# Performance work log

Measured on AMD Instinct MI355X. Metric: run time of the kernel, lower is better.

The kernel has to match this reference:

```python
import jax, jax.numpy as jnp
import numpy as np

LOCAL_HEADS = 8
GLOBAL_HEADS = 4
HEAD_DIM = 16  # dim // local_heads


def setup_inputs() -> dict:
    key = jax.random.key(0)
    ks = jax.random.split(key, 6)
    B, N, C = 8, 1024, 128
    gdim = HEAD_DIM * GLOBAL_HEADS  # 64
    return {
        "x": jax.random.normal(ks[0], (B, N, C), dtype=jnp.float32),
        "masks": jax.random.uniform(ks[1], (N, N, 3), dtype=jnp.float32),
        "Wq": jax.random.normal(ks[2], (gdim, C), dtype=jnp.float32) * 0.05,
        "Wk": jax.random.normal(ks[3], (gdim, C), dtype=jnp.float32) * 0.05,
        "Wv": jax.random.normal(ks[4], (C, C), dtype=jnp.float32) * 0.05,
        "mask_proj": jax.random.normal(ks[5], (3, GLOBAL_HEADS * LOCAL_HEADS), dtype=jnp.float32),
    }


def reference(x, masks, Wq, Wk, Wv, mask_proj):
    B, N, C = x.shape
    # projections (torch Linear: y = x @ W.T)
    q = (x @ Wq.T).reshape(B, N, GLOBAL_HEADS, HEAD_DIM)   # [B,N,G,hd]
    k = (x @ Wk.T).reshape(B, N, GLOBAL_HEADS, HEAD_DIM)
    v = (x @ Wv.T).reshape(B, N, LOCAL_HEADS, HEAD_DIM)    # [B,N,L,hd]
    # raw global-head scores: [B,G,N,N]  (no 1/sqrt(d) scaling in original)
    attn = jnp.einsum('bigd,bjgd->bgij', q, k)
    # learned mask mixing: masks [N,N,3] @ mask_proj [3, G*L] -> [N,N,G,L]
    mw = (masks @ mask_proj).reshape(N, N, GLOBAL_HEADS, LOCAL_HEADS)
    # mix global heads into local heads: [B,L,N,N]
    scores = jnp.einsum('bgij,ijgl->blij', attn, mw)
    probs = jax.nn.softmax(scores, axis=-1)               # over keys j
    out = jnp.einsum('blij,bjld->bild', probs, v)         # [B,N,L,hd]
    return out.reshape(B, N, C)
```

## Files before the change

### kernel.cpp

```cpp
#include <hip/hip_runtime.h>

#define BB 8
#define NN 1024
#define CC 128
#define GG 4
#define LL 8
#define GD 64

typedef __attribute__((ext_vector_type(8))) short short8;
typedef __attribute__((ext_vector_type(4))) short short4v;
typedef __attribute__((ext_vector_type(4))) float floatx4;

__device__ __forceinline__ short f2b(float f) {
  union { float f; unsigned u; } c; c.f = f;
  unsigned u = c.u;
  return (short)((u + 0x7FFFu + ((u >> 16) & 1u)) >> 16);
}
__device__ __forceinline__ float b2f(short s) {
  union { unsigned u; float f; } c; c.u = ((unsigned)(unsigned short)s) << 16;
  return c.f;
}
__device__ __forceinline__ void split2(float v, short& hi, short& lo) {
  short h = f2b(v);
  hi = h;
  lo = f2b(v - b2f(h));
}

#if __has_builtin(__builtin_amdgcn_cvt_pk_bf16_f32)
__device__ __forceinline__ unsigned pk2(float a, float b) {
  auto r = __builtin_amdgcn_cvt_pk_bf16_f32(a, b);
  unsigned u; __builtin_memcpy(&u, &r, 4); return u;
}
#else
__device__ __forceinline__ unsigned pk2(float a, float b) {
  return (unsigned)(unsigned short)f2b(a) | ((unsigned)(unsigned short)f2b(b) << 16);
}
#endif

#if __has_builtin(__builtin_amdgcn_exp2f)
#define EXP2(x) __builtin_amdgcn_exp2f(x)
#else
#define EXP2(x) exp2f(x)
#endif

#define BHP 136

__global__ __launch_bounds__(256) void proj_kernel(
    const float* __restrict__ x, const float* __restrict__ Wq,
    const float* __restrict__ Wk, const float* __restrict__ Wv,
    short* __restrict__ qb, short* __restrict__ kb, short* __restrict__ vtb)
{
  __shared__ short bh[64 * BHP];
  __shared__ short bl[64 * BHP];
  const int t = threadIdx.x;
  const int nt = blockIdx.x & 3;
  const int mt = blockIdx.x >> 2;
  const int w = t >> 6;
  const int lane = t & 63;
  const int ln = lane & 15;
  const int hq = lane >> 4;
  const int arow = mt * 64 + w * 16 + ln;

  const float* wbase = (nt == 0) ? Wq : (nt == 1) ? Wk : (Wv + (nt - 2) * 64 * 128);

  {
    int r = t >> 2, c0 = (t & 3) * 32;
    const float* src = wbase + r * 128 + c0;
    #pragma unroll
    for (int z8 = 0; z8 < 4; ++z8) {
      float4 u0 = *(const float4*)(src + z8 * 8);
      float4 u1 = *(const float4*)(src + z8 * 8 + 4);
      float uv[8] = {u0.x,u0.y,u0.z,u0.w,u1.x,u1.y,u1.z,u1.w};
      union { short s[8]; short8 v; } H, L;
      #pragma unroll
      for (int z = 0; z < 8; ++z) split2(uv[z], H.s[z], L.s[z]);
      *(short8*)(bh + r * BHP + c0 + z8 * 8) = H.v;
      *(short8*)(bl + r * BHP + c0 + z8 * 8) = L.v;
    }
  }
  __syncthreads();

  const floatx4 zf = {0.f, 0.f, 0.f, 0.f};
  floatx4 acc[4] = {zf, zf, zf, zf};

  #pragma unroll
  for (int kc = 0; kc < 4; ++kc) {
    const float* xp = x + (long)arow * 128 + kc * 32 + hq * 8;
    float4 a0 = *(const float4*)xp;
    float4 a1 = *(const float4*)(xp + 4);
    union { short s[8]; short8 v; } Ah, Al;
    float av[8] = {a0.x,a0.y,a0.z,a0.w,a1.x,a1.y,a1.z,a1.w};
    #pragma unroll
    for (int z = 0; z < 8; ++z) split2(av[z], Ah.s[z], Al.s[z]);
    #pragma unroll
    for (int ns = 0; ns < 4; ++ns) {
      short8 Bh = *(const short8*)(bh + (ns * 16 + ln) * BHP + kc * 32 + hq * 8);
      short8 Bl = *(const short8*)(bl + (ns * 16 + ln) * BHP + kc * 32 + hq * 8);
      acc[ns] = __builtin_amdgcn_mfma_f32_16x16x32_bf16(Ah.v, Bh, acc[ns], 0,0,0);
      acc[ns] = __builtin_amdgcn_mfma_f32_16x16x32_bf16(Al.v, Bh, acc[ns], 0,0,0);
      acc[ns] = __builtin_amdgcn_mfma_f32_16x16x32_bf16(Ah.v, Bl, acc[ns], 0,0,0);
    }
  }

  if (nt < 2) {
    short* dst = (nt == 0) ? qb : kb;
    #pragma unroll
    for (int ns = 0; ns < 4; ++ns) {
      int col = ns * 16 + ln;
      #pragma unroll
      for (int reg = 0; reg < 4; ++reg) {
        int row = mt * 64 + w * 16 + hq * 4 + reg;
        dst[(long)row * 64 + col] = f2b(acc[ns][reg]);
      }
    }
  } else {
    int b = mt >> 4;
    int tok = (mt * 64 + w * 16 + hq * 4) & 1023;
    #pragma unroll
    for (int ns = 0; ns < 4; ++ns) {
      int cv = (nt - 2) * 64 + ns * 16 + ln;
      union { short s[4]; short4v v; } o;
      #pragma unroll
      for (int reg = 0; reg < 4; ++reg) o.s[reg] = f2b(acc[ns][reg]);
      *(short4v*)(vtb + ((long)b * CC + cv) * NN + tok) = o.v;
    }
  }
}

#define IT 16
#define JT 64
#define SPLIT 2
#define JSPAN 512
#define NTL 8
#define ARP 260
#define MRP 196

__global__ __launch_bounds__(256, 3) void attn_kernel(
    const short* __restrict__ qb, const short* __restrict__ kb,
    const short* __restrict__ vtb, const float* __restrict__ masks,
    const float* __restrict__ mask_proj,
    float* __restrict__ pnum, float* __restrict__ pden)
{
  __shared__ float arec[IT * ARP];
  __shared__ float mrec[IT * MRP];

  const int t = threadIdx.x;
  const int sp = blockIdx.x & 1;
  const int itile = (blockIdx.x >> 1) & 63;
  const int b = blockIdx.x >> 7;
  const int i0 = itile * IT;

  const int w = t >> 6;
  const int lane = t & 63;
  const int ln = lane & 15;
  const int hq = lane >> 4;
  const int l0 = 2 * w, l1 = 2 * w + 1;

  short8 qf;
  {
    union { short s[8]; short8 v; } qq;
    #pragma unroll
    for (int z = 0; z < 8; ++z) qq.s[z] = 0;
    if (hq < 2)
      qq.v = *(const short8*)(qb + ((long)(b * NN + i0 + ln)) * GD + w * 16 + hq * 8);
    qf = qq.v;
  }
  const float LOG2E = 1.44269504088896340736f;
  float ycA[3][4], ycB[3][4];
  #pragma unroll
  for (int m = 0; m < 3; ++m)
    #pragma unroll
    for (int g = 0; g < 4; ++g) {
      ycA[m][g] = mask_proj[m * 32 + g * 8 + l0] * LOG2E;
      ycB[m][g] = mask_proj[m * 32 + g * 8 + l1] * LOG2E;
    }

  const floatx4 zf = {0.f, 0.f, 0.f, 0.f};
  floatx4 pv0 = zf, pv1 = zf;
  float den0 = 0.f, den1 = 0.f;

  const short* kbase = kb + (long)b * NN * GD;
  const short* v0base = vtb + ((long)b * CC + l0 * 16 + ln) * NN;
  const short* v1base = vtb + ((long)b * CC + l1 * 16 + ln) * NN;

  for (int jt = 0; jt < NTL; ++jt) {
    const int j0 = sp * JSPAN + jt * JT;
    __syncthreads();

    #pragma unroll
    for (int it2 = 0; it2 < 3; ++it2) {
      int f = t + it2 * 256;
      int ii = f / 48;
      int rem = f - ii * 48;
      *(float4*)(mrec + ii * MRP + rem * 4) =
        *(const float4*)(masks + (long)(i0 + ii) * (NN * 3) + (long)j0 * 3 + rem * 4);
    }
    #pragma unroll
    for (int jsub = 0; jsub < 4; ++jsub) {
      union { short s[8]; short8 v; } kk;
      #pragma unroll
      for (int z = 0; z < 8; ++z) kk.s[z] = 0;
      if (hq < 2)
        kk.v = *(const short8*)(kbase + (long)(j0 + jsub * 16 + ln) * GD + w * 16 + hq * 8);
      floatx4 at = __builtin_amdgcn_mfma_f32_16x16x32_bf16(qf, kk.v, zf, 0, 0, 0);
      float* ab = arec + (jsub * 16 + ln) * 4 + w;
      #pragma unroll
      for (int reg = 0; reg < 4; ++reg)
        ab[(hq * 4 + reg) * ARP] = at[reg];
    }
    __syncthreads();

    #pragma unroll
    for (int mf = 0; mf < 2; ++mf) {
      float mku[24];
      {
        const float* mb = mrec + ln * MRP + mf * 96 + hq * 24;
        #pragma unroll
        for (int q4 = 0; q4 < 6; ++q4)
          *(float4*)(mku + q4 * 4) = *(const float4*)(mb + q4 * 4);
      }
      short8 vf0 = *(const short8*)(v0base + j0 + mf * 32 + hq * 8);
      short8 vf1 = *(const short8*)(v1base + j0 + mf * 32 + hq * 8);
      const float* arA = arec + ln * ARP + (mf * 32 + hq * 8) * 4;
      union { unsigned u[4]; short8 v; } p0, p1;
      #pragma unroll
      for (int zp = 0; zp < 4; ++zp) {
        float eA[2], eB[2];
        #pragma unroll
        for (int zz = 0; zz < 2; ++zz) {
          int z = zp * 2 + zz;
          floatx4 a4 = *(const floatx4*)(arA + z * 4);
          float m0 = mku[z * 3], m1 = mku[z * 3 + 1], m2 = mku[z * 3 + 2];
          float wA0 = m0*ycA[0][0] + m1*ycA[1][0] + m2*ycA[2][0];
          float wA1 = m0*ycA[0][1] + m1*ycA[1][1] + m2*ycA[2][1];
          float wA2 = m0*ycA[0][2] + m1*ycA[1][2] + m2*ycA[2][2];
          float wA3 = m0*ycA[0][3] + m1*ycA[1][3] + m2*ycA[2][3];
          float wB0 = m0*ycB[0][0] + m1*ycB[1][0] + m2*ycB[2][0];
          float wB1 = m0*ycB[0][1] + m1*ycB[1][1] + m2*ycB[2][1];
          float wB2 = m0*ycB[0][2] + m1*ycB[1][2] + m2*ycB[2][2];
          float wB3 = m0*ycB[0][3] + m1*ycB[1][3] + m2*ycB[2][3];
          float sA = a4[0]*wA0 + a4[1]*wA1 + a4[2]*wA2 + a4[3]*wA3;
          float sB = a4[0]*wB0 + a4[1]*wB1 + a4[2]*wB2 + a4[3]*wB3;
          eA[zz] = EXP2(sA);
          eB[zz] = EXP2(sB);
        }
        den0 += eA[0] + eA[1];
        den1 += eB[0] + eB[1];
        p0.u[zp] = pk2(eA[0], eA[1]);
        p1.u[zp] = pk2(eB[0], eB[1]);
      }
      pv0 = __builtin_amdgcn_mfma_f32_16x16x32_bf16(p0.v, vf0, pv0, 0, 0, 0);
      pv1 = __builtin_amdgcn_mfma_f32_16x16x32_bf16(p1.v, vf1, pv1, 0, 0, 0);
    }
  }

  #pragma unroll
  for (int reg = 0; reg < 4; ++reg) {
    long row = ((long)(sp * BB + b)) * NN + i0 + hq * 4 + reg;
    pnum[row * CC + l0 * 16 + ln] = pv0[reg];
    pnum[row * CC + l1 * 16 + ln] = pv1[reg];
  }
  den0 += __shfl_xor(den0, 16, 64);
  den0 += __shfl_xor(den0, 32, 64);
  den1 += __shfl_xor(den1, 16, 64);
  den1 += __shfl_xor(den1, 32, 64);
  if (hq == 0) {
    long drow = ((long)(sp * BB + b)) * NN + i0 + ln;
    pden[drow * LL + l0] = den0;
    pden[drow * LL + l1] = den1;
  }
}

__global__ __launch_bounds__(256) void reduce_kernel(
    const float* __restrict__ pnum, const float* __restrict__ pden,
    float* __restrict__ out)
{
  int e4 = blockIdx.x * 256 + threadIdx.x;
  int bi = e4 >> 5;
  int l = (e4 & 31) >> 2;
  const float4* p4 = (const float4*)pnum;
  float4 n0 = p4[e4];
  float4 n1 = p4[e4 + (BB * NN * CC / 4)];
  float den = pden[(long)bi * LL + l] + pden[((long)BB * NN + bi) * LL + l];
  float inv = 1.0f / den;
  float4 o;
  o.x = (n0.x + n1.x) * inv;
  o.y = (n0.y + n1.y) * inv;
  o.z = (n0.z + n1.z) * inv;
  o.w = (n0.w + n1.w) * inv;
  ((float4*)out)[e4] = o;
}

extern "C" void kernel_launch(void* const* d_in, const int* in_sizes, int n_in,
                              void* d_out, int out_size, void* d_ws, size_t ws_size,
                              hipStream_t stream) {
  const float* x         = (const float*)d_in[0];
  const float* masks     = (const float*)d_in[1];
  const float* Wq        = (const float*)d_in[2];
  const float* Wk        = (const float*)d_in[3];
  const float* Wv        = (const float*)d_in[4];
  const float* mask_proj = (const float*)d_in[5];
  float* out = (float*)d_out;

  char* wsB = (char*)d_ws;
  short* qb   = (short*)(wsB);
  short* kb   = (short*)(wsB + (1l << 20));
  short* vtb  = (short*)(wsB + (2l << 20));
  float* pnum = (float*)(wsB + (4l << 20));
  float* pden = (float*)(wsB + (12l << 20));

  proj_kernel<<<512, 256, 0, stream>>>(x, Wq, Wk, Wv, qb, kb, vtb);
  attn_kernel<<<BB * (NN / IT) * SPLIT, 256, 0, stream>>>(qb, kb, vtb, masks,
                                                          mask_proj, pnum, pden);
  reduce_kernel<<<(BB * NN * CC / 4) / 256, 256, 0, stream>>>(pnum, pden, out);
}
```

Baseline: 128.9 us.

## Register-prefetch next mask and K tiles, raise attention occupancy hint

```diff
diff --git a/kernel.cpp b/kernel.cpp
--- a/kernel.cpp
+++ b/kernel.cpp
@@ -135,7 +135,7 @@
 #define ARP 260
 #define MRP 196
 
-__global__ __launch_bounds__(256, 3) void attn_kernel(
+__global__ __launch_bounds__(256, 4) void attn_kernel(
     const short* __restrict__ qb, const short* __restrict__ kb,
     const short* __restrict__ vtb, const float* __restrict__ masks,
     const float* __restrict__ mask_proj,
@@ -183,30 +183,58 @@
   const short* v0base = vtb + ((long)b * CC + l0 * 16 + ln) * NN;
   const short* v1base = vtb + ((long)b * CC + l1 * 16 + ln) * NN;
 
+  const int mf0 = t;
+  const int mii0 = mf0 / 48, mrem0 = mf0 - mii0 * 48;
+  const int mf1 = t + 256;
+  const int mii1 = mf1 / 48, mrem1 = mf1 - mii1 * 48;
+  const int mf2 = t + 512;
+  const int mii2 = mf2 / 48, mrem2 = mf2 - mii2 * 48;
+
+  float4 mstage[3];
+  short8 kst[4];
+  {
+    union { short s[8]; short8 v; } z8;
+    #pragma unroll
+    for (int z = 0; z < 8; ++z) z8.s[z] = 0;
+    kst[0] = z8.v; kst[1] = z8.v; kst[2] = z8.v; kst[3] = z8.v;
+    const int j0p = sp * JSPAN;
+    mstage[0] = *(const float4*)(masks + (long)(i0 + mii0) * (NN * 3) + (long)j0p * 3 + mrem0 * 4);
+    mstage[1] = *(const float4*)(masks + (long)(i0 + mii1) * (NN * 3) + (long)j0p * 3 + mrem1 * 4);
+    mstage[2] = *(const float4*)(masks + (long)(i0 + mii2) * (NN * 3) + (long)j0p * 3 + mrem2 * 4);
+    if (hq < 2) {
+      #pragma unroll
+      for (int jsub = 0; jsub < 4; ++jsub)
+        kst[jsub] = *(const short8*)(kbase + (long)(j0p + jsub * 16 + ln) * GD + w * 16 + hq * 8);
+    }
+  }
+
   for (int jt = 0; jt < NTL; ++jt) {
     const int j0 = sp * JSPAN + jt * JT;
     __syncthreads();
 
-    #pragma unroll
-    for (int it2 = 0; it2 < 3; ++it2) {
-      int f = t + it2 * 256;
-      int ii = f / 48;
-      int rem = f - ii * 48;
-      *(float4*)(mrec + ii * MRP + rem * 4) =
-        *(const float4*)(masks + (long)(i0 + ii) * (NN * 3) + (long)j0 * 3 + rem * 4);
-    }
+    *(float4*)(mrec + mii0 * MRP + mrem0 * 4) = mstage[0];
+    *(float4*)(mrec + mii1 * MRP + mrem1 * 4) = mstage[1];
+    *(float4*)(mrec + mii2 * MRP + mrem2 * 4) = mstage[2];
+
     #pragma unroll
     for (int jsub = 0; jsub < 4; ++jsub) {
-      union { short s[8]; short8 v; } kk;
-      #pragma unroll
-      for (int z = 0; z < 8; ++z) kk.s[z] = 0;
-      if (hq < 2)
-        kk.v = *(const short8*)(kbase + (long)(j0 + jsub * 16 + ln) * GD + w * 16 + hq * 8);
-      floatx4 at = __builtin_amdgcn_mfma_f32_16x16x32_bf16(qf, kk.v, zf, 0, 0, 0);
+      floatx4 at = __builtin_amdgcn_mfma_f32_16x16x32_bf16(qf, kst[jsub], zf, 0, 0, 0);
       float* ab = arec + (jsub * 16 + ln) * 4 + w;
       #pragma unroll
       for (int reg = 0; reg < 4; ++reg)
         ab[(hq * 4 + reg) * ARP] = at[reg];
+    }
+
+    {
+      const int jn = sp * JSPAN + ((jt + 1) & (NTL - 1)) * JT;
+      mstage[0] = *(const float4*)(masks + (long)(i0 + mii0) * (NN * 3) + (long)jn * 3 + mrem0 * 4);
+      mstage[1] = *(const float4*)(masks + (long)(i0 + mii1) * (NN * 3) + (long)jn * 3 + mrem1 * 4);
+      mstage[2] = *(const float4*)(masks + (long)(i0 + mii2) * (NN * 3) + (long)jn * 3 + mrem2 * 4);
+      if (hq < 2) {
+        #pragma unroll
+        for (int jsub = 0; jsub < 4; ++jsub)
+          kst[jsub] = *(const short8*)(kbase + (long)(jn + jsub * 16 + ln) * GD + w * 16 + hq * 8);
+      }
     }
     __syncthreads();
 
```

After: 156.8 us. +21.7%, slower.

## Double-buffer QK scores in LDS and read masks directly from global

Applied to the files above, without the earlier changes.

```diff
diff --git a/kernel.cpp b/kernel.cpp
--- a/kernel.cpp
+++ b/kernel.cpp
@@ -133,7 +133,6 @@
 #define JSPAN 512
 #define NTL 8
 #define ARP 260
-#define MRP 196
 
 __global__ __launch_bounds__(256, 3) void attn_kernel(
     const short* __restrict__ qb, const short* __restrict__ kb,
@@ -141,8 +140,7 @@
     const float* __restrict__ mask_proj,
     float* __restrict__ pnum, float* __restrict__ pden)
 {
-  __shared__ float arec[IT * ARP];
-  __shared__ float mrec[IT * MRP];
+  __shared__ float arec[2 * IT * ARP];
 
   const int t = threadIdx.x;
   const int sp = blockIdx.x & 1;
@@ -182,77 +180,79 @@
   const short* kbase = kb + (long)b * NN * GD;
   const short* v0base = vtb + ((long)b * CC + l0 * 16 + ln) * NN;
   const short* v1base = vtb + ((long)b * CC + l1 * 16 + ln) * NN;
-
-  for (int jt = 0; jt < NTL; ++jt) {
-    const int j0 = sp * JSPAN + jt * JT;
+  const float* mrowbase = masks + (long)(i0 + ln) * (NN * 3);
+
+#define QK_PHASE(J0, ABASE) { \
+    _Pragma("unroll") \
+    for (int jsub = 0; jsub < 4; ++jsub) { \
+      union { short s[8]; short8 v; } kk; \
+      _Pragma("unroll") \
+      for (int z = 0; z < 8; ++z) kk.s[z] = 0; \
+      if (hq < 2) \
+        kk.v = *(const short8*)(kbase + (long)((J0) + jsub * 16 + ln) * GD + w * 16 + hq * 8); \
+      floatx4 at = __builtin_amdgcn_mfma_f32_16x16x32_bf16(qf, kk.v, zf, 0, 0, 0); \
+      float* ab = (ABASE) + (jsub * 16 + ln) * 4 + w; \
+      _Pragma("unroll") \
+      for (int reg = 0; reg < 4; ++reg) \
+        ab[(hq * 4 + reg) * ARP] = at[reg]; \
+    } }
+
+#define MIX_PHASE(J0, ABASE) { \
+    _Pragma("unroll") \
+    for (int mf = 0; mf < 2; ++mf) { \
+      float mku[24]; \
+      { \
+        const float* mb = mrowbase + (long)((J0) + mf * 32 + hq * 8) * 3; \
+        _Pragma("unroll") \
+        for (int q4 = 0; q4 < 6; ++q4) \
+          *(float4*)(mku + q4 * 4) = *(const float4*)(mb + q4 * 4); \
+      } \
+      short8 vf0 = *(const short8*)(v0base + (J0) + mf * 32 + hq * 8); \
+      short8 vf1 = *(const short8*)(v1base + (J0) + mf * 32 + hq * 8); \
+      const float* arA = (ABASE) + ln * ARP + (mf * 32 + hq * 8) * 4; \
+      union { unsigned u[4]; short8 v; } p0, p1; \
+      _Pragma("unroll") \
+      for (int zp = 0; zp < 4; ++zp) { \
+        float eA[2], eB[2]; \
+        _Pragma("unroll") \
+        for (int zz = 0; zz < 2; ++zz) { \
+          int z = zp * 2 + zz; \
+          floatx4 a4 = *(const floatx4*)(arA + z * 4); \
+          float m0 = mku[z * 3], m1 = mku[z * 3 + 1], m2 = mku[z * 3 + 2]; \
+          float wA0 = m0*ycA[0][0] + m1*ycA[1][0] + m2*ycA[2][0]; \
+          float wA1 = m0*ycA[0][1] + m1*ycA[1][1] + m2*ycA[2][1]; \
+          float wA2 = m0*ycA[0][2] + m1*ycA[1][2] + m2*ycA[2][2]; \
+          float wA3 = m0*ycA[0][3] + m1*ycA[1][3] + m2*ycA[2][3]; \
+          float wB0 = m0*ycB[0][0] + m1*ycB[1][0] + m2*ycB[2][0]; \
+          float wB1 = m0*ycB[0][1] + m1*ycB[1][1] + m2*ycB[2][1]; \
+          float wB2 = m0*ycB[0][2] + m1*ycB[1][2] + m2*ycB[2][2]; \
+          float wB3 = m0*ycB[0][3] + m1*ycB[1][3] + m2*ycB[2][3]; \
+          float sA = a4[0]*wA0 + a4[1]*wA1 + a4[2]*wA2 + a4[3]*wA3; \
+          float sB = a4[0]*wB0 + a4[1]*wB1 + a4[2]*wB2 + a4[3]*wB3; \
+          eA[zz] = EXP2(sA); \
+          eB[zz] = EXP2(sB); \
+        } \
+        den0 += eA[0] + eA[1]; \
+        den1 += eB[0] + eB[1]; \
+        p0.u[zp] = pk2(eA[0], eA[1]); \
+        p1.u[zp] = pk2(eB[0], eB[1]); \
+      } \
+      pv0 = __builtin_amdgcn_mfma_f32_16x16x32_bf16(p0.v, vf0, pv0, 0, 0, 0); \
+      pv1 = __builtin_amdgcn_mfma_f32_16x16x32_bf16(p1.v, vf1, pv1, 0, 0, 0); \
+    } }
+
+  QK_PHASE(sp * JSPAN, arec)
+  __syncthreads();
+  for (int jt = 1; jt < NTL; ++jt) {
+    float* qbuf = arec + (jt & 1) * (IT * ARP);
+    const float* mbuf = arec + ((jt & 1) ^ 1) * (IT * ARP);
+    const int jq = sp * JSPAN + jt * JT;
+    const int jm = jq - JT;
+    QK_PHASE(jq, qbuf)
+    MIX_PHASE(jm, mbuf)
     __syncthreads();
-
-    #pragma unroll
-    for (int it2 = 0; it2 < 3; ++it2) {
-      int f = t + it2 * 256;
-      int ii = f / 48;
-      int rem = f - ii * 48;
-      *(float4*)(mrec + ii * MRP + rem * 4) =
-        *(const float4*)(masks + (long)(i0 + ii) * (NN * 3) + (long)j0 * 3 + rem * 4);
-    }
-    #pragma unroll
-    for (int jsub = 0; jsub < 4; ++jsub) {
-      union { short s[8]; short8 v; } kk;
-      #pragma unroll
-      for (int z = 0; z < 8; ++z) kk.s[z] = 0;
-      if (hq < 2)
-        kk.v = *(const short8*)(kbase + (long)(j0 + jsub * 16 + ln) * GD + w * 16 + hq * 8);
-      floatx4 at = __builtin_amdgcn_mfma_f32_16x16x32_bf16(qf, kk.v, zf, 0, 0, 0);
-      float* ab = arec + (jsub * 16 + ln) * 4 + w;
-      #pragma unroll
-      for (int reg = 0; reg < 4; ++reg)
-        ab[(hq * 4 + reg) * ARP] = at[reg];
-    }
-    __syncthreads();
-
-    #pragma unroll
-    for (int mf = 0; mf < 2; ++mf) {
-      float mku[24];
-      {
-        const float* mb = mrec + ln * MRP + mf * 96 + hq * 24;
-        #pragma unroll
-        for (int q4 = 0; q4 < 6; ++q4)
-          *(float4*)(mku + q4 * 4) = *(const float4*)(mb + q4 * 4);
-      }
-      short8 vf0 = *(const short8*)(v0base + j0 + mf * 32 + hq * 8);
-      short8 vf1 = *(const short8*)(v1base + j0 + mf * 32 + hq * 8);
-      const float* arA = arec + ln * ARP + (mf * 32 + hq * 8) * 4;
-      union { unsigned u[4]; short8 v; } p0, p1;
-      #pragma unroll
-      for (int zp = 0; zp < 4; ++zp) {
-        float eA[2], eB[2];
-        #pragma unroll
-        for (int zz = 0; zz < 2; ++zz) {
-          int z = zp * 2 + zz;
-          floatx4 a4 = *(const floatx4*)(arA + z * 4);
-          float m0 = mku[z * 3], m1 = mku[z * 3 + 1], m2 = mku[z * 3 + 2];
-          float wA0 = m0*ycA[0][0] + m1*ycA[1][0] + m2*ycA[2][0];
-          float wA1 = m0*ycA[0][1] + m1*ycA[1][1] + m2*ycA[2][1];
-          float wA2 = m0*ycA[0][2] + m1*ycA[1][2] + m2*ycA[2][2];
-          float wA3 = m0*ycA[0][3] + m1*ycA[1][3] + m2*ycA[2][3];
-          float wB0 = m0*ycB[0][0] + m1*ycB[1][0] + m2*ycB[2][0];
-          float wB1 = m0*ycB[0][1] + m1*ycB[1][1] + m2*ycB[2][1];
-          float wB2 = m0*ycB[0][2] + m1*ycB[1][2] + m2*ycB[2][2];
-          float wB3 = m0*ycB[0][3] + m1*ycB[1][3] + m2*ycB[2][3];
-          float sA = a4[0]*wA0 + a4[1]*wA1 + a4[2]*wA2 + a4[3]*wA3;
-          float sB = a4[0]*wB0 + a4[1]*wB1 + a4[2]*wB2 + a4[3]*wB3;
-          eA[zz] = EXP2(sA);
-          eB[zz] = EXP2(sB);
-        }
-        den0 += eA[0] + eA[1];
-        den1 += eB[0] + eB[1];
-        p0.u[zp] = pk2(eA[0], eA[1]);
-        p1.u[zp] = pk2(eB[0], eB[1]);
-      }
-      pv0 = __builtin_amdgcn_mfma_f32_16x16x32_bf16(p0.v, vf0, pv0, 0, 0, 0);
-      pv1 = __builtin_amdgcn_mfma_f32_16x16x32_bf16(p1.v, vf1, pv1, 0, 0, 0);
-    }
-  }
+  }
+  MIX_PHASE(sp * JSPAN + (NTL - 1) * JT, arec + ((NTL - 1) & 1) * (IT * ARP))
 
   #pragma unroll
   for (int reg = 0; reg < 4; ++reg) {
```

Result: slower. 163.5 us (+26.8%).
